# Performance work log

Hardware: AMD Instinct MI355X
Metric: run time of the kernel (lower is better)

## Reference

```python
import jax, jax.numpy as jnp
import numpy as np

EMBED, HIDDEN, VOCAB = 256, 512, 32000
B, T = 16, 63  # captions length; total steps per item = T+1


def setup_inputs() -> dict:
    key = jax.random.key(0)
    ks = jax.random.split(key, 9)
    s = 0.05
    return {
        "features": jax.random.normal(ks[0], (B, EMBED), jnp.float32),
        "captions": jax.random.randint(ks[1], (B, T), 0, VOCAB, jnp.int32),
        "emb": jax.random.normal(ks[2], (VOCAB, EMBED), jnp.float32) * s,
        "W_ih": jax.random.normal(ks[3], (4 * HIDDEN, EMBED), jnp.float32) * s,
        "W_hh": jax.random.normal(ks[4], (4 * HIDDEN, HIDDEN), jnp.float32) * s,
        "b_ih": jax.random.normal(ks[5], (4 * HIDDEN,), jnp.float32) * s,
        "b_hh": jax.random.normal(ks[6], (4 * HIDDEN,), jnp.float32) * s,
        "W_out": jax.random.normal(ks[7], (VOCAB, HIDDEN), jnp.float32) * s,
        "b_out": jax.random.normal(ks[8], (VOCAB,), jnp.float32) * s,
    }


def reference(features, captions, emb, W_ih, W_hh, b_ih, b_hh, W_out, b_out):
    H = W_hh.shape[1]
    embeds = emb[captions]  # [B, T, E]
    # inputs = cat(features.unsqueeze(1), embeds, dim=1) -> [B, T+1, E]
    inputs = jnp.concatenate([features[:, None, :], embeds], axis=1)
    # The torch loop threads self.hidden across batch items -> one long
    # sequential LSTM over B*(T+1) steps starting from zero state.
    xs = inputs.reshape(-1, inputs.shape[-1])  # [B*(T+1), E]
    # precompute input projections for all steps (one big GEMM)
    x_proj = xs @ W_ih.T + b_ih + b_hh  # [S, 4H]

    def cell(carry, xp):
        h, c = carry
        gates = xp + h @ W_hh.T  # [4H]
        i, f, g, o = jnp.split(gates, 4)
        i = jax.nn.sigmoid(i)
        f = jax.nn.sigmoid(f)
        g = jnp.tanh(g)
        o = jax.nn.sigmoid(o)
        c = f * c + i * g
        h = o * jnp.tanh(c)
        return (h, c), h

    h0 = jnp.zeros((H,), xs.dtype)
    c0 = jnp.zeros((H,), xs.dtype)
    _, hs = jax.lax.scan(cell, (h0, c0), x_proj)  # [S, H]
    logits = hs @ W_out.T + b_out  # [S, V]
    probs = jax.nn.softmax(logits, axis=-1)
    return probs.reshape(inputs.shape[0], inputs.shape[1], -1)  # [B, T+1, V]
```

## Files before the change

kernel.cpp:

```cpp
#include <hip/hip_runtime.h>
#include <cstdint>
#include <cstddef>

#define EMBED  256
#define HIDDEN 512
#define VOCAB  32000
#define BATCH  16
#define TCAP   63
#define STEPS  1024
#define GROWS  2048

#define WS_HBUF  0
#define WS_HS32  8192
#define WS_HSBF  2105344
#define WS_WB    3153920
#define WS_XPOFF (24u * 1024u * 1024u)
#define WS_NEED  36708352ull
#define WB_HEAD_ELEMS 12582912

typedef __bf16 bf16x8 __attribute__((ext_vector_type(8)));
typedef float  f32x4  __attribute__((ext_vector_type(4)));

__device__ __forceinline__ float sigmoid_f(float x) {
    return 1.0f / (1.0f + __expf(-x));
}
__device__ __forceinline__ float tanh_f(float x) {
    float a = fabsf(x);
    float e = __expf(-2.0f * a);
    float r = (1.0f - e) / (1.0f + e);
    return copysignf(r, x);
}
__device__ __forceinline__ float sel4(float a0, float a1, float a2, float a3, int j) {
    float lo = (j & 1) ? a1 : a0;
    float hi = (j & 1) ? a3 : a2;
    return (j & 2) ? hi : lo;
}
__device__ __forceinline__ unsigned short f2bf_u16(float f) {
    union { float f; unsigned u; } v; v.f = f;
    unsigned r = v.u + 0x7fffu + ((v.u >> 16) & 1u);
    return (unsigned short)(r >> 16);
}

__global__ __launch_bounds__(256) void xproj_kernel(
    const float* __restrict__ features,
    const int*   __restrict__ captions,
    const float* __restrict__ emb,
    const float* __restrict__ W_ih,
    const float* __restrict__ b_ih,
    const float* __restrict__ b_hh,
    float* __restrict__ xp)
{
    __shared__ float As[64][65];
    __shared__ float Bs[64][65];
    const int tid = threadIdx.x;
    const int tx = tid & 15, ty = tid >> 4;
    const int r0 = blockIdx.x * 64;
    const int s0 = blockIdx.y * 64;
    float accv[4][4] = {};

    for (int k0 = 0; k0 < EMBED; k0 += 64) {
#pragma unroll
        for (int i = 0; i < 4; ++i) {
            const int idx = tid + i * 256;
            const int row = idx >> 4, q = idx & 15;
            const int s = s0 + row, sb = s >> 6, st = s & 63;
            const float* xr = (st == 0)
                ? (features + (size_t)sb * EMBED)
                : (emb + (size_t)captions[sb * TCAP + st - 1] * EMBED);
            const float4 a = *(const float4*)(xr + k0 + q * 4);
            As[row][q * 4 + 0] = a.x; As[row][q * 4 + 1] = a.y;
            As[row][q * 4 + 2] = a.z; As[row][q * 4 + 3] = a.w;
            const float4 b = *(const float4*)(W_ih + (size_t)(r0 + row) * EMBED + k0 + q * 4);
            Bs[row][q * 4 + 0] = b.x; Bs[row][q * 4 + 1] = b.y;
            Bs[row][q * 4 + 2] = b.z; Bs[row][q * 4 + 3] = b.w;
        }
        __syncthreads();
#pragma unroll 16
        for (int kk = 0; kk < 64; ++kk) {
            float av[4], bv[4];
#pragma unroll
            for (int i = 0; i < 4; ++i) av[i] = As[ty * 4 + i][kk];
#pragma unroll
            for (int j = 0; j < 4; ++j) bv[j] = Bs[tx * 4 + j][kk];
#pragma unroll
            for (int i = 0; i < 4; ++i)
#pragma unroll
                for (int j = 0; j < 4; ++j)
                    accv[i][j] = fmaf(av[i], bv[j], accv[i][j]);
        }
        __syncthreads();
    }
#pragma unroll
    for (int j = 0; j < 4; ++j) {
        const int r = r0 + tx * 4 + j;
        const float bb = b_ih[r] + b_hh[r];
#pragma unroll
        for (int i = 0; i < 4; ++i)
            xp[(size_t)(s0 + ty * 4 + i) * GROWS + r] = accv[i][j] + bb;
    }
}

__global__ __launch_bounds__(256, 1) void lstm_scan_kernel(
    const float* __restrict__ W_hh,
    const float* __restrict__ xp,
    unsigned long long* __restrict__ hbuf,
    float* __restrict__ hs32,
    __bf16* __restrict__ hsbf,
    const float* __restrict__ W_out,
    unsigned short* __restrict__ Wb,
    const int wbf)
{
    const int tid = threadIdx.x;

    if (blockIdx.x >= 32) {
        const int cb = blockIdx.x - 32;
        const int stride = 224 * 256 * 4;
        for (int i = (cb * 256 + tid) * 4; i < WB_HEAD_ELEMS; i += stride) {
            const float4 v = *(const float4*)(W_out + i);
            ushort4 o;
            o.x = f2bf_u16(v.x); o.y = f2bf_u16(v.y);
            o.z = f2bf_u16(v.z); o.w = f2bf_u16(v.w);
            *(ushort4*)(Wb + i) = o;
        }
        return;
    }

    const int rg  = tid >> 6;
    const int kc  = tid & 63;
    const int w   = blockIdx.x * 4 + rg;
    const int j0  = w * 4;

    __shared__ float hlds[2][HIDDEN];

    const int t_own  = ((kc & 1) << 1) | ((kc >> 1) & 1);
    const int jj_own = (((kc >> 2) & 1) << 1) | ((kc >> 3) & 1);
    const int row_own = t_own * HIDDEN + j0 + jj_own;

    float Whh[4][4][8];
#pragma unroll
    for (int t = 0; t < 4; ++t) {
#pragma unroll
        for (int jj = 0; jj < 4; ++jj) {
            const int row = t * HIDDEN + j0 + jj;
            const float4* ph = (const float4*)(W_hh + (size_t)row * HIDDEN + kc * 8);
            const float4 h0 = ph[0], h1 = ph[1];
            Whh[t][jj][0] = h0.x; Whh[t][jj][1] = h0.y; Whh[t][jj][2] = h0.z; Whh[t][jj][3] = h0.w;
            Whh[t][jj][4] = h1.x; Whh[t][jj][5] = h1.y; Whh[t][jj][6] = h1.z; Whh[t][jj][7] = h1.w;
        }
    }

    float c_state = 0.0f;
    float xpv_next = xp[row_own];
    const int qi = rg * 128 + kc * 2;

    for (int s = 0; s < STEPS; ++s) {
        const int p = s & 1;
        const unsigned expect = (unsigned)s;
        const float xpv = xpv_next;

        const int sn = (s + 1 < STEPS) ? (s + 1) : (STEPS - 1);
        xpv_next = xp[(size_t)sn * GROWS + row_own];

        const unsigned long long* hb = hbuf + (size_t)p * HIDDEN + qi;
        unsigned long long va, vb;
        for (;;) {
            va = __hip_atomic_load(hb,     __ATOMIC_RELAXED, __HIP_MEMORY_SCOPE_AGENT);
            vb = __hip_atomic_load(hb + 1, __ATOMIC_RELAXED, __HIP_MEMORY_SCOPE_AGENT);
            const bool ok = ((unsigned)(va >> 32) == expect) &
                            ((unsigned)(vb >> 32) == expect);
            if (__all((int)ok)) break;
            __builtin_amdgcn_s_sleep(1);
        }
        hlds[p][qi]     = __uint_as_float((unsigned)(va & 0xffffffffULL));
        hlds[p][qi + 1] = __uint_as_float((unsigned)(vb & 0xffffffffULL));
        __syncthreads();

        float hreg[8];
        {
            const float4 a = *(const float4*)&hlds[p][kc * 8];
            const float4 b = *(const float4*)&hlds[p][kc * 8 + 4];
            hreg[0] = a.x; hreg[1] = a.y; hreg[2] = a.z; hreg[3] = a.w;
            hreg[4] = b.x; hreg[5] = b.y; hreg[6] = b.z; hreg[7] = b.w;
        }

        float acc[16];
#pragma unroll
        for (int t = 0; t < 4; ++t) {
#pragma unroll
            for (int jj = 0; jj < 4; ++jj) {
                float a = Whh[t][jj][0] * hreg[0];
#pragma unroll
                for (int kk = 1; kk < 8; ++kk)
                    a = fmaf(Whh[t][jj][kk], hreg[kk], a);
                acc[t * 4 + jj] = a;
            }
        }

#pragma unroll
        for (int i = 0; i < 8; ++i) {
            const float send = (kc & 1) ? acc[i] : acc[i + 8];
            const float keep = (kc & 1) ? acc[i + 8] : acc[i];
            acc[i] = keep + __shfl_xor(send, 1, 64);
        }
#pragma unroll
        for (int i = 0; i < 4; ++i) {
            const float send = (kc & 2) ? acc[i] : acc[i + 4];
            const float keep = (kc & 2) ? acc[i + 4] : acc[i];
            acc[i] = keep + __shfl_xor(send, 2, 64);
        }
#pragma unroll
        for (int i = 0; i < 2; ++i) {
            const float send = (kc & 4) ? acc[i] : acc[i + 2];
            const float keep = (kc & 4) ? acc[i + 2] : acc[i];
            acc[i] = keep + __shfl_xor(send, 4, 64);
        }
        {
            const float send = (kc & 8) ? acc[0] : acc[1];
            const float keep = (kc & 8) ? acc[1] : acc[0];
            acc[0] = keep + __shfl_xor(send, 8, 64);
        }
        float a = acc[0];
        a += __shfl_xor(a, 16, 64);
        a += __shfl_xor(a, 32, 64);
        a += xpv;

        const float g00 = a;
        const float g01 = __shfl_xor(a, 1, 64);
        const float g10 = __shfl_xor(a, 2, 64);
        const float g11 = __shfl_xor(g01, 2, 64);
        float gi = sel4(g00, g10, g01, g11, t_own);
        float gf = sel4(g00, g10, g01, g11, t_own ^ 1);
        float gg = sel4(g00, g10, g01, g11, t_own ^ 2);
        float go = sel4(g00, g10, g01, g11, t_own ^ 3);

        gi = sigmoid_f(gi);
        gf = sigmoid_f(gf);
        gg = tanh_f(gg);
        go = sigmoid_f(go);
        c_state = gf * c_state + gi * gg;
        const float hnew = go * tanh_f(c_state);

        if ((kc & 0x33) == 0) {
            const int j = j0 + jj_own;
            const unsigned long long pack =
                ((unsigned long long)(unsigned)(s + 1) << 32) |
                (unsigned long long)__float_as_uint(hnew);
            __hip_atomic_store(hbuf + (size_t)((s + 1) & 1) * HIDDEN + j, pack,
                               __ATOMIC_RELAXED, __HIP_MEMORY_SCOPE_AGENT);
            hs32[(size_t)s * HIDDEN + j] = hnew;
            if (wbf) hsbf[(size_t)s * HIDDEN + j] = (__bf16)hnew;
        }
    }
}

__global__ __launch_bounds__(256) void convert_tail_kernel(
    const float* __restrict__ W, unsigned short* __restrict__ Wb,
    int lo, int n)
{
    const int stride = gridDim.x * blockDim.x * 4;
    for (int i = lo + (blockIdx.x * blockDim.x + threadIdx.x) * 4; i < n; i += stride) {
        const float4 v = *(const float4*)(W + i);
        ushort4 o;
        o.x = f2bf_u16(v.x); o.y = f2bf_u16(v.y);
        o.z = f2bf_u16(v.z); o.w = f2bf_u16(v.w);
        *(ushort4*)(Wb + i) = o;
    }
}

__global__ __launch_bounds__(256) void logits_mfma_kernel(
    const __bf16* __restrict__ A,
    const __bf16* __restrict__ B,
    const float* __restrict__ b_out,
    float* __restrict__ out)
{
    __shared__ char AsR[16384];
    __shared__ char BsR[16384];
    const int tid  = threadIdx.x;
    const int lane = tid & 63;
    const int wave = tid >> 6;
    const int wm = (wave >> 1) * 64;
    const int wn = (wave & 1) * 64;
    const int n0 = blockIdx.x * 128;
    const int m0 = blockIdx.y * 128;

    f32x4 acc[4][4] = {};

    for (int k0 = 0; k0 < HIDDEN; k0 += 64) {
        if (k0) __syncthreads();
#pragma unroll
        for (int i = 0; i < 4; ++i) {
            const int o   = (tid + i * 256) << 4;
            const int row = o >> 7;
            const int cb  = o & 127;
            const int sc  = cb ^ ((row & 7) << 4);
            const bf16x8 av = *(const bf16x8*)(A + (size_t)(m0 + row) * HIDDEN + k0 + (cb >> 1));
            const bf16x8 bv = *(const bf16x8*)(B + (size_t)(n0 + row) * HIDDEN + k0 + (cb >> 1));
            *(bf16x8*)(AsR + row * 128 + sc) = av;
            *(bf16x8*)(BsR + row * 128 + sc) = bv;
        }
        __syncthreads();
#pragma unroll
        for (int ks = 0; ks < 2; ++ks) {
            const int kb = ks * 64 + ((lane >> 4) << 4);
            bf16x8 af[4], bfr[4];
#pragma unroll
            for (int mi = 0; mi < 4; ++mi) {
                const int r = wm + mi * 16 + (lane & 15);
                af[mi] = *(const bf16x8*)(AsR + r * 128 + (kb ^ ((r & 7) << 4)));
            }
#pragma unroll
            for (int ni = 0; ni < 4; ++ni) {
                const int r = wn + ni * 16 + (lane & 15);
                bfr[ni] = *(const bf16x8*)(BsR + r * 128 + (kb ^ ((r & 7) << 4)));
            }
#pragma unroll
            for (int mi = 0; mi < 4; ++mi)
#pragma unroll
                for (int ni = 0; ni < 4; ++ni)
                    acc[mi][ni] = __builtin_amdgcn_mfma_f32_16x16x32_bf16(
                        af[mi], bfr[ni], acc[mi][ni], 0, 0, 0);
        }
    }

#pragma unroll
    for (int ni = 0; ni < 4; ++ni) {
        const int col = n0 + wn + ni * 16 + (lane & 15);
        const float bo = b_out[col];
#pragma unroll
        for (int mi = 0; mi < 4; ++mi) {
            const int r0 = m0 + wm + mi * 16 + ((lane >> 4) << 2);
#pragma unroll
            for (int qq = 0; qq < 4; ++qq)
                out[(size_t)(r0 + qq) * VOCAB + col] = acc[mi][ni][qq] + bo;
        }
    }
}

__global__ __launch_bounds__(256) void logits_kernel(
    const float* __restrict__ hs,
    const float* __restrict__ W_out,
    const float* __restrict__ b_out,
    float* __restrict__ out)
{
    __shared__ float As[64][65];
    __shared__ float Bs[64][65];
    const int tid = threadIdx.x;
    const int tx = tid & 15, ty = tid >> 4;
    const int v0 = blockIdx.x * 64;
    const int s0 = blockIdx.y * 64;
    float accv[4][4] = {};

    for (int k0 = 0; k0 < HIDDEN; k0 += 64) {
#pragma unroll
        for (int i = 0; i < 4; ++i) {
            const int idx = tid + i * 256;
            const int r = idx >> 4, q = idx & 15;
            const float4 a = *(const float4*)(hs + (size_t)(s0 + r) * HIDDEN + k0 + q * 4);
            As[r][q * 4 + 0] = a.x; As[r][q * 4 + 1] = a.y;
            As[r][q * 4 + 2] = a.z; As[r][q * 4 + 3] = a.w;
            const float4 b = *(const float4*)(W_out + (size_t)(v0 + r) * HIDDEN + k0 + q * 4);
            Bs[r][q * 4 + 0] = b.x; Bs[r][q * 4 + 1] = b.y;
            Bs[r][q * 4 + 2] = b.z; Bs[r][q * 4 + 3] = b.w;
        }
        __syncthreads();
#pragma unroll 16
        for (int kk = 0; kk < 64; ++kk) {
            float av[4], bv[4];
#pragma unroll
            for (int i = 0; i < 4; ++i) av[i] = As[ty * 4 + i][kk];
#pragma unroll
            for (int j = 0; j < 4; ++j) bv[j] = Bs[tx * 4 + j][kk];
#pragma unroll
            for (int i = 0; i < 4; ++i)
#pragma unroll
                for (int j = 0; j < 4; ++j)
                    accv[i][j] = fmaf(av[i], bv[j], accv[i][j]);
        }
        __syncthreads();
    }
#pragma unroll
    for (int i = 0; i < 4; ++i) {
        const int s = s0 + ty * 4 + i;
#pragma unroll
        for (int j = 0; j < 4; ++j) {
            const int v = v0 + tx * 4 + j;
            out[(size_t)s * VOCAB + v] = accv[i][j] + b_out[v];
        }
    }
}

__global__ __launch_bounds__(256) void softmax_kernel(float* __restrict__ out)
{
    const int row = blockIdx.x;
    float* p = out + (size_t)row * VOCAB;
    const int tid = threadIdx.x;
    __shared__ float redm[4];
    __shared__ float reds[4];

    float m = -3.402823466e38f;
    for (int idx = tid * 4; idx < VOCAB; idx += 1024) {
        const float4 v = *(const float4*)(p + idx);
        m = fmaxf(m, fmaxf(fmaxf(v.x, v.y), fmaxf(v.z, v.w)));
    }
#pragma unroll
    for (int d = 1; d < 64; d <<= 1) m = fmaxf(m, __shfl_xor(m, d, 64));
    if ((tid & 63) == 0) redm[tid >> 6] = m;
    __syncthreads();
    m = fmaxf(fmaxf(redm[0], redm[1]), fmaxf(redm[2], redm[3]));

    float sum = 0.f;
    for (int idx = tid * 4; idx < VOCAB; idx += 1024) {
        const float4 v = *(const float4*)(p + idx);
        sum += __expf(v.x - m) + __expf(v.y - m) + __expf(v.z - m) + __expf(v.w - m);
    }
#pragma unroll
    for (int d = 1; d < 64; d <<= 1) sum += __shfl_xor(sum, d, 64);
    if ((tid & 63) == 0) reds[tid >> 6] = sum;
    __syncthreads();
    sum = reds[0] + reds[1] + reds[2] + reds[3];
    const float inv = 1.0f / sum;

    for (int idx = tid * 4; idx < VOCAB; idx += 1024) {
        const float4 v = *(const float4*)(p + idx);
        float4 o;
        o.x = __expf(v.x - m) * inv;
        o.y = __expf(v.y - m) * inv;
        o.z = __expf(v.z - m) * inv;
        o.w = __expf(v.w - m) * inv;
        *(float4*)(p + idx) = o;
    }
}

extern "C" void kernel_launch(void* const* d_in, const int* in_sizes, int n_in,
                              void* d_out, int out_size, void* d_ws, size_t ws_size,
                              hipStream_t stream)
{
    const float* features = (const float*)d_in[0];
    const int*   captions = (const int*)d_in[1];
    const float* emb      = (const float*)d_in[2];
    const float* W_ih     = (const float*)d_in[3];
    const float* W_hh     = (const float*)d_in[4];
    const float* b_ih     = (const float*)d_in[5];
    const float* b_hh     = (const float*)d_in[6];
    const float* W_out    = (const float*)d_in[7];
    const float* b_out    = (const float*)d_in[8];
    float* out = (float*)d_out;

    char* ws = (char*)d_ws;
    unsigned long long* hbuf = (unsigned long long*)(ws + WS_HBUF);
    float*              hs32 = (float*)(ws + WS_HS32);
    __bf16*             hsbf = (__bf16*)(ws + WS_HSBF);
    __bf16*             Wb   = (__bf16*)(ws + WS_WB);
    const bool mfma_ok = ws_size >= WS_NEED;
    float* xpb = mfma_ok ? (float*)(ws + WS_WB + WS_XPOFF) : (float*)(ws + WS_WB);

    hipMemsetAsync(d_ws, 0, 8192, stream);

    xproj_kernel<<<dim3(GROWS / 64, STEPS / 64), 256, 0, stream>>>(
        features, captions, emb, W_ih, b_ih, b_hh, xpb);

    lstm_scan_kernel<<<mfma_ok ? 256 : 32, 256, 0, stream>>>(
        W_hh, xpb, hbuf, hs32, hsbf,
        W_out, (unsigned short*)Wb, mfma_ok ? 1 : 0);

    if (mfma_ok) {
        convert_tail_kernel<<<512, 256, 0, stream>>>(
            W_out, (unsigned short*)Wb, WB_HEAD_ELEMS, VOCAB * HIDDEN);
        logits_mfma_kernel<<<dim3(VOCAB / 128, STEPS / 128), 256, 0, stream>>>(
            hsbf, Wb, b_out, out);
    } else {
        logits_kernel<<<dim3(VOCAB / 64, STEPS / 64), 256, 0, stream>>>(
            hs32, W_out, b_out, out);
    }
    softmax_kernel<<<STEPS, 256, 0, stream>>>(out);
}
```

Baseline: 2.170 ms.

## Co-locate LSTM scan blocks on one XCD and use L2-local fast handoff

Scan blocks are now assigned dynamically. Blocks that start on XCD 0 claim the 32 recurrent slots first, so all scan workgroups can share one L2 cache. When every slot holder sits on the same XCD, hidden-state exchange goes through a separate buffer using plain vectorized loads with sc0 and volatile stores. This avoids device-scope atomic round trips, and a bounded spin falls back to the agent-scope atomic buffer. The change depends on non-portable hardware register reads and L2 coherence assumptions, and it adds a startup rendezvous. The fp32 hidden-state store is skipped when the bf16 path is active.

```diff
diff --git a/kernel.cpp b/kernel.cpp
--- a/kernel.cpp
+++ b/kernel.cpp
@@ -9,17 +9,21 @@
 #define TCAP   63
 #define STEPS  1024
 #define GROWS  2048
-
-#define WS_HBUF  0
-#define WS_HS32  8192
-#define WS_HSBF  2105344
-#define WS_WB    3153920
+#define NCONV  224
+
+#define WS_FAST  0
+#define WS_SLOW  8192
+#define WS_CTRS  16384
+#define WS_HS32  16640
+#define WS_HSBF  (16640 + 2097152)
+#define WS_WB    (16640 + 3145728)
 #define WS_XPOFF (24u * 1024u * 1024u)
-#define WS_NEED  36708352ull
+#define WS_NEED  (3162368ull + 33554432ull)
 #define WB_HEAD_ELEMS 12582912
 
 typedef __bf16 bf16x8 __attribute__((ext_vector_type(8)));
 typedef float  f32x4  __attribute__((ext_vector_type(4)));
+typedef unsigned int u32x4v __attribute__((ext_vector_type(4)));
 
 __device__ __forceinline__ float sigmoid_f(float x) {
     return 1.0f / (1.0f + __expf(-x));
@@ -103,7 +107,9 @@
 __global__ __launch_bounds__(256, 1) void lstm_scan_kernel(
     const float* __restrict__ W_hh,
     const float* __restrict__ xp,
-    unsigned long long* __restrict__ hbuf,
+    unsigned long long* __restrict__ fastb,
+    unsigned long long* __restrict__ slowb,
+    unsigned* __restrict__ ctrs,
     float* __restrict__ hs32,
     __bf16* __restrict__ hsbf,
     const float* __restrict__ W_out,
@@ -111,11 +117,57 @@
     const int wbf)
 {
     const int tid = threadIdx.x;
-
-    if (blockIdx.x >= 32) {
-        const int cb = blockIdx.x - 32;
-        const int stride = 224 * 256 * 4;
-        for (int i = (cb * 256 + tid) * 4; i < WB_HEAD_ELEMS; i += stride) {
+    __shared__ int sh_slot, sh_uni, sh_ticket;
+
+    if (tid == 0) {
+        unsigned xcd;
+        asm volatile("s_getreg_b32 %0, hwreg(HW_REG_XCC_ID)" : "=s"(xcd));
+        int id = -1;
+        if (xcd == 0u) {
+            const unsigned c = __hip_atomic_fetch_add(ctrs + 0, 1u,
+                __ATOMIC_RELAXED, __HIP_MEMORY_SCOPE_AGENT);
+            if (c < 32u) id = (int)c;
+        }
+        if (id < 0) {
+            for (int t = 0; t < 24; ++t) {
+                if (__hip_atomic_load(ctrs + 0, __ATOMIC_RELAXED,
+                                      __HIP_MEMORY_SCOPE_AGENT) >= 32u) break;
+                __builtin_amdgcn_s_sleep(127);
+            }
+            if (__hip_atomic_load(ctrs + 0, __ATOMIC_RELAXED,
+                                  __HIP_MEMORY_SCOPE_AGENT) < 32u) {
+                const unsigned c = __hip_atomic_fetch_add(ctrs + 0, 1u,
+                    __ATOMIC_RELAXED, __HIP_MEMORY_SCOPE_AGENT);
+                if (c < 32u) id = (int)c;
+            }
+        }
+        int uni = 0;
+        if (id >= 0) {
+            __hip_atomic_fetch_add(ctrs + 1, 1u | ((xcd == 0u) ? 0u : 0x10000u),
+                                   __ATOMIC_RELAXED, __HIP_MEMORY_SCOPE_AGENT);
+            unsigned cd;
+            for (;;) {
+                cd = __hip_atomic_load(ctrs + 1, __ATOMIC_RELAXED,
+                                       __HIP_MEMORY_SCOPE_AGENT);
+                if ((cd & 0xffffu) >= 32u) break;
+                __builtin_amdgcn_s_sleep(2);
+            }
+            uni = ((cd >> 16) == 0u) ? 1 : 0;
+        } else {
+            sh_ticket = (int)__hip_atomic_fetch_add(ctrs + 2, 1u,
+                __ATOMIC_RELAXED, __HIP_MEMORY_SCOPE_AGENT);
+        }
+        sh_slot = id;
+        sh_uni = uni;
+    }
+    __syncthreads();
+    const int slot = sh_slot;
+
+    if (slot < 0) {
+        if (!wbf) return;
+        const int ticket = sh_ticket;
+        const int stride = NCONV * 256 * 4;
+        for (int i = (ticket * 256 + tid) * 4; i < WB_HEAD_ELEMS; i += stride) {
             const float4 v = *(const float4*)(W_out + i);
             ushort4 o;
             o.x = f2bf_u16(v.x); o.y = f2bf_u16(v.y);
@@ -125,9 +177,11 @@
         return;
     }
 
+    bool usefast = (sh_uni != 0);
+
     const int rg  = tid >> 6;
     const int kc  = tid & 63;
-    const int w   = blockIdx.x * 4 + rg;
+    const int w   = slot * 4 + rg;
     const int j0  = w * 4;
 
     __shared__ float hlds[2][HIDDEN];
@@ -161,18 +215,36 @@
         const int sn = (s + 1 < STEPS) ? (s + 1) : (STEPS - 1);
         xpv_next = xp[(size_t)sn * GROWS + row_own];
 
-        const unsigned long long* hb = hbuf + (size_t)p * HIDDEN + qi;
-        unsigned long long va, vb;
-        for (;;) {
-            va = __hip_atomic_load(hb,     __ATOMIC_RELAXED, __HIP_MEMORY_SCOPE_AGENT);
-            vb = __hip_atomic_load(hb + 1, __ATOMIC_RELAXED, __HIP_MEMORY_SCOPE_AGENT);
-            const bool ok = ((unsigned)(va >> 32) == expect) &
-                            ((unsigned)(vb >> 32) == expect);
-            if (__all((int)ok)) break;
-            __builtin_amdgcn_s_sleep(1);
-        }
-        hlds[p][qi]     = __uint_as_float((unsigned)(va & 0xffffffffULL));
-        hlds[p][qi + 1] = __uint_as_float((unsigned)(vb & 0xffffffffULL));
+        unsigned d0, d1;
+        const unsigned long long fa = (unsigned long long)(fastb + (size_t)p * HIDDEN + qi);
+        if (usefast) {
+            int it = 0;
+            for (;;) {
+                u32x4v v;
+                asm volatile("global_load_dwordx4 %0, %1, off sc0\n\t"
+                             "s_waitcnt vmcnt(0)"
+                             : "=v"(v) : "v"(fa) : "memory");
+                const bool ok = (v.y == expect) & (v.w == expect);
+                if (__all((int)ok)) { d0 = v.x; d1 = v.z; break; }
+                if (++it >= 2048) { usefast = false; break; }
+            }
+        }
+        if (!usefast) {
+            const unsigned long long* hb = slowb + (size_t)p * HIDDEN + qi;
+            unsigned long long va, vb;
+            for (;;) {
+                va = __hip_atomic_load(hb,     __ATOMIC_RELAXED, __HIP_MEMORY_SCOPE_AGENT);
+                vb = __hip_atomic_load(hb + 1, __ATOMIC_RELAXED, __HIP_MEMORY_SCOPE_AGENT);
+                const bool ok = ((unsigned)(va >> 32) == expect) &
+                                ((unsigned)(vb >> 32) == expect);
+                if (__all((int)ok)) break;
+                __builtin_amdgcn_s_sleep(1);
+            }
+            d0 = (unsigned)(va & 0xffffffffULL);
+            d1 = (unsigned)(vb & 0xffffffffULL);
+        }
+        hlds[p][qi]     = __uint_as_float(d0);
+        hlds[p][qi + 1] = __uint_as_float(d1);
         __syncthreads();
 
         float hreg[8];
@@ -240,15 +312,17 @@
         c_state = gf * c_state + gi * gg;
         const float hnew = go * tanh_f(c_state);
 
+        const int q = (s + 1) & 1;
         if ((kc & 0x33) == 0) {
             const int j = j0 + jj_own;
             const unsigned long long pack =
                 ((unsigned long long)(unsigned)(s + 1) << 32) |
                 (unsigned long long)__float_as_uint(hnew);
-            __hip_atomic_store(hbuf + (size_t)((s + 1) & 1) * HIDDEN + j, pack,
+            *(volatile unsigned long long*)(fastb + (size_t)q * HIDDEN + j) = pack;
+            __hip_atomic_store(slowb + (size_t)q * HIDDEN + j, pack,
                                __ATOMIC_RELAXED, __HIP_MEMORY_SCOPE_AGENT);
-            hs32[(size_t)s * HIDDEN + j] = hnew;
             if (wbf) hsbf[(size_t)s * HIDDEN + j] = (__bf16)hnew;
+            else     hs32[(size_t)s * HIDDEN + j] = hnew;
         }
     }
 }
@@ -447,20 +521,22 @@
     float* out = (float*)d_out;
 
     char* ws = (char*)d_ws;
-    unsigned long long* hbuf = (unsigned long long*)(ws + WS_HBUF);
-    float*              hs32 = (float*)(ws + WS_HS32);
-    __bf16*             hsbf = (__bf16*)(ws + WS_HSBF);
-    __bf16*             Wb   = (__bf16*)(ws + WS_WB);
+    unsigned long long* fastb = (unsigned long long*)(ws + WS_FAST);
+    unsigned long long* slowb = (unsigned long long*)(ws + WS_SLOW);
+    unsigned*           ctrs  = (unsigned*)(ws + WS_CTRS);
+    float*              hs32  = (float*)(ws + WS_HS32);
+    __bf16*             hsbf  = (__bf16*)(ws + WS_HSBF);
+    __bf16*             Wb    = (__bf16*)(ws + WS_WB);
     const bool mfma_ok = ws_size >= WS_NEED;
     float* xpb = mfma_ok ? (float*)(ws + WS_WB + WS_XPOFF) : (float*)(ws + WS_WB);
 
-    hipMemsetAsync(d_ws, 0, 8192, stream);
+    hipMemsetAsync(d_ws, 0, WS_HS32, stream);
 
     xproj_kernel<<<dim3(GROWS / 64, STEPS / 64), 256, 0, stream>>>(
         features, captions, emb, W_ih, b_ih, b_hh, xpb);
 
-    lstm_scan_kernel<<<mfma_ok ? 256 : 32, 256, 0, stream>>>(
-        W_hh, xpb, hbuf, hs32, hsbf,
+    lstm_scan_kernel<<<256, 256, 0, stream>>>(
+        W_hh, xpb, fastb, slowb, ctrs, hs32, hsbf,
         W_out, (unsigned short*)Wb, mfma_ok ? 1 : 0);
 
     if (mfma_ok) {
```

New measurement: 2.414 ms. 1.11x slower.

## Replicate per-block hidden-state mailboxes and move weight conversion into xproj kernel

Applied to the files above, without the earlier changes.

The LSTM scan now has each block poll its own replicated copy of the hidden-state buffer using one 16-byte cache-bypassing load. Previously all 32 blocks polled a shared 2-slot buffer with two atomic loads and a sleep. Producers write each value to two mailbox replicas via lane shuffles, so the stores are spread across lanes. The W_out bf16 head conversion moves from extra scan-kernel blocks into extra blocks of the input-projection kernel, so the scan runs without co-resident converter traffic. This aims to cut per-step sync latency and memory contention on the serial critical path, at the cost of more store traffic per step and inline asm relying on sc0/sc1 coherence semantics.

```diff
diff --git a/kernel.cpp b/kernel.cpp
--- a/kernel.cpp
+++ b/kernel.cpp
@@ -10,16 +10,17 @@
 #define STEPS  1024
 #define GROWS  2048
 
-#define WS_HBUF  0
-#define WS_HS32  8192
-#define WS_HSBF  2105344
-#define WS_WB    3153920
+#define WS_PBUF  0
+#define WS_HSBF  262144
+#define WS_HS32  1310720
+#define WS_WB    3407872
 #define WS_XPOFF (24u * 1024u * 1024u)
-#define WS_NEED  36708352ull
+#define WS_NEED  36962304ull
 #define WB_HEAD_ELEMS 12582912
 
 typedef __bf16 bf16x8 __attribute__((ext_vector_type(8)));
 typedef float  f32x4  __attribute__((ext_vector_type(4)));
+typedef unsigned int u32x4v __attribute__((ext_vector_type(4)));
 
 __device__ __forceinline__ float sigmoid_f(float x) {
     return 1.0f / (1.0f + __expf(-x));
@@ -35,24 +36,47 @@
     float hi = (j & 1) ? a3 : a2;
     return (j & 2) ? hi : lo;
 }
+__device__ __forceinline__ int sel4i(int a0, int a1, int a2, int a3, int j) {
+    int lo = (j & 1) ? a1 : a0;
+    int hi = (j & 1) ? a3 : a2;
+    return (j & 2) ? hi : lo;
+}
 __device__ __forceinline__ unsigned short f2bf_u16(float f) {
     union { float f; unsigned u; } v; v.f = f;
     unsigned r = v.u + 0x7fffu + ((v.u >> 16) & 1u);
     return (unsigned short)(r >> 16);
 }
 
-__global__ __launch_bounds__(256) void xproj_kernel(
+__global__ __launch_bounds__(256) void xproj_conv_kernel(
     const float* __restrict__ features,
     const int*   __restrict__ captions,
     const float* __restrict__ emb,
     const float* __restrict__ W_ih,
     const float* __restrict__ b_ih,
     const float* __restrict__ b_hh,
-    float* __restrict__ xp)
-{
+    float* __restrict__ xp,
+    const float* __restrict__ W_out,
+    unsigned short* __restrict__ Wb,
+    const int wbf)
+{
+    const int tid = threadIdx.x;
+
+    if (blockIdx.y >= 16) {
+        if (!wbf) return;
+        const int cid = (blockIdx.y - 16) * 32 + blockIdx.x;
+        const int stride = 256 * 256 * 4;
+        for (int i = (cid * 256 + tid) * 4; i < WB_HEAD_ELEMS; i += stride) {
+            const float4 v = *(const float4*)(W_out + i);
+            ushort4 o;
+            o.x = f2bf_u16(v.x); o.y = f2bf_u16(v.y);
+            o.z = f2bf_u16(v.z); o.w = f2bf_u16(v.w);
+            *(ushort4*)(Wb + i) = o;
+        }
+        return;
+    }
+
     __shared__ float As[64][65];
     __shared__ float Bs[64][65];
-    const int tid = threadIdx.x;
     const int tx = tid & 15, ty = tid >> 4;
     const int r0 = blockIdx.x * 64;
     const int s0 = blockIdx.y * 64;
@@ -103,31 +127,16 @@
 __global__ __launch_bounds__(256, 1) void lstm_scan_kernel(
     const float* __restrict__ W_hh,
     const float* __restrict__ xp,
-    unsigned long long* __restrict__ hbuf,
+    unsigned long long* __restrict__ pbuf,
     float* __restrict__ hs32,
     __bf16* __restrict__ hsbf,
-    const float* __restrict__ W_out,
-    unsigned short* __restrict__ Wb,
     const int wbf)
 {
     const int tid = threadIdx.x;
-
-    if (blockIdx.x >= 32) {
-        const int cb = blockIdx.x - 32;
-        const int stride = 224 * 256 * 4;
-        for (int i = (cb * 256 + tid) * 4; i < WB_HEAD_ELEMS; i += stride) {
-            const float4 v = *(const float4*)(W_out + i);
-            ushort4 o;
-            o.x = f2bf_u16(v.x); o.y = f2bf_u16(v.y);
-            o.z = f2bf_u16(v.z); o.w = f2bf_u16(v.w);
-            *(ushort4*)(Wb + i) = o;
-        }
-        return;
-    }
-
     const int rg  = tid >> 6;
     const int kc  = tid & 63;
-    const int w   = blockIdx.x * 4 + rg;
+    const int g   = blockIdx.x;
+    const int w   = g * 4 + rg;
     const int j0  = w * 4;
 
     __shared__ float hlds[2][HIDDEN];
@@ -135,6 +144,12 @@
     const int t_own  = ((kc & 1) << 1) | ((kc >> 1) & 1);
     const int jj_own = (((kc >> 2) & 1) << 1) | ((kc >> 3) & 1);
     const int row_own = t_own * HIDDEN + j0 + jj_own;
+
+    const int e_pub = kc & 3;
+    const int src_lane = sel4i(0, 8, 4, 12, e_pub);
+    const int c0 = kc >> 2;
+    unsigned long long* const mc0 = pbuf + (size_t)c0 * 2 * HIDDEN + j0 + e_pub;
+    unsigned long long* const mc1 = mc0 + (size_t)16 * 2 * HIDDEN;
 
     float Whh[4][4][8];
 #pragma unroll
@@ -150,29 +165,29 @@
     }
 
     float c_state = 0.0f;
-    float xpv_next = xp[row_own];
+    float xpv = xp[row_own];
+    float xpv_next;
     const int qi = rg * 128 + kc * 2;
 
     for (int s = 0; s < STEPS; ++s) {
         const int p = s & 1;
         const unsigned expect = (unsigned)s;
-        const float xpv = xpv_next;
-
-        const int sn = (s + 1 < STEPS) ? (s + 1) : (STEPS - 1);
-        xpv_next = xp[(size_t)sn * GROWS + row_own];
-
-        const unsigned long long* hb = hbuf + (size_t)p * HIDDEN + qi;
-        unsigned long long va, vb;
+
+        const unsigned long long fa =
+            (unsigned long long)(pbuf + ((size_t)g * 2 + p) * HIDDEN + qi);
+        unsigned d0, d1;
         for (;;) {
-            va = __hip_atomic_load(hb,     __ATOMIC_RELAXED, __HIP_MEMORY_SCOPE_AGENT);
-            vb = __hip_atomic_load(hb + 1, __ATOMIC_RELAXED, __HIP_MEMORY_SCOPE_AGENT);
-            const bool ok = ((unsigned)(va >> 32) == expect) &
-                            ((unsigned)(vb >> 32) == expect);
-            if (__all((int)ok)) break;
-            __builtin_amdgcn_s_sleep(1);
-        }
-        hlds[p][qi]     = __uint_as_float((unsigned)(va & 0xffffffffULL));
-        hlds[p][qi + 1] = __uint_as_float((unsigned)(vb & 0xffffffffULL));
+            u32x4v v;
+            asm volatile("global_load_dwordx4 %0, %1, off sc0 sc1\n\t"
+                         "s_waitcnt vmcnt(0)"
+                         : "=&v"(v) : "v"(fa) : "memory");
+            if (__all((int)((v.y == expect) & (v.w == expect)))) {
+                d0 = v.x; d1 = v.z; break;
+            }
+        }
+
+        hlds[p][qi]     = __uint_as_float(d0);
+        hlds[p][qi + 1] = __uint_as_float(d1);
         __syncthreads();
 
         float hreg[8];
@@ -182,6 +197,9 @@
             hreg[0] = a.x; hreg[1] = a.y; hreg[2] = a.z; hreg[3] = a.w;
             hreg[4] = b.x; hreg[5] = b.y; hreg[6] = b.z; hreg[7] = b.w;
         }
+
+        const int sn = (s + 1 < STEPS) ? (s + 1) : (STEPS - 1);
+        xpv_next = xp[(size_t)sn * GROWS + row_own];
 
         float acc[16];
 #pragma unroll
@@ -240,16 +258,23 @@
         c_state = gf * c_state + gi * gg;
         const float hnew = go * tanh_f(c_state);
 
+        const int q = (s + 1) & 1;
+        const float hsrc = __shfl(hnew, src_lane, 64);
+        const unsigned long long pack =
+            ((unsigned long long)(unsigned)(s + 1) << 32) |
+            (unsigned long long)__float_as_uint(hsrc);
+        __hip_atomic_store(mc0 + (size_t)q * HIDDEN, pack,
+                           __ATOMIC_RELAXED, __HIP_MEMORY_SCOPE_AGENT);
+        __hip_atomic_store(mc1 + (size_t)q * HIDDEN, pack,
+                           __ATOMIC_RELAXED, __HIP_MEMORY_SCOPE_AGENT);
+
         if ((kc & 0x33) == 0) {
             const int j = j0 + jj_own;
-            const unsigned long long pack =
-                ((unsigned long long)(unsigned)(s + 1) << 32) |
-                (unsigned long long)__float_as_uint(hnew);
-            __hip_atomic_store(hbuf + (size_t)((s + 1) & 1) * HIDDEN + j, pack,
-                               __ATOMIC_RELAXED, __HIP_MEMORY_SCOPE_AGENT);
-            hs32[(size_t)s * HIDDEN + j] = hnew;
             if (wbf) hsbf[(size_t)s * HIDDEN + j] = (__bf16)hnew;
-        }
+            else     hs32[(size_t)s * HIDDEN + j] = hnew;
+        }
+
+        xpv = xpv_next;
     }
 }
 
@@ -447,21 +472,21 @@
     float* out = (float*)d_out;
 
     char* ws = (char*)d_ws;
-    unsigned long long* hbuf = (unsigned long long*)(ws + WS_HBUF);
+    unsigned long long* pbuf = (unsigned long long*)(ws + WS_PBUF);
+    __bf16*             hsbf = (__bf16*)(ws + WS_HSBF);
     float*              hs32 = (float*)(ws + WS_HS32);
-    __bf16*             hsbf = (__bf16*)(ws + WS_HSBF);
     __bf16*             Wb   = (__bf16*)(ws + WS_WB);
     const bool mfma_ok = ws_size >= WS_NEED;
     float* xpb = mfma_ok ? (float*)(ws + WS_WB + WS_XPOFF) : (float*)(ws + WS_WB);
 
-    hipMemsetAsync(d_ws, 0, 8192, stream);
-
-    xproj_kernel<<<dim3(GROWS / 64, STEPS / 64), 256, 0, stream>>>(
-        features, captions, emb, W_ih, b_ih, b_hh, xpb);
-
-    lstm_scan_kernel<<<mfma_ok ? 256 : 32, 256, 0, stream>>>(
-        W_hh, xpb, hbuf, hs32, hsbf,
+    hipMemsetAsync(d_ws, 0, 32 * 2 * HIDDEN * 8, stream);
+
+    xproj_conv_kernel<<<dim3(32, 24), 256, 0, stream>>>(
+        features, captions, emb, W_ih, b_ih, b_hh, xpb,
         W_out, (unsigned short*)Wb, mfma_ok ? 1 : 0);
+
+    lstm_scan_kernel<<<32, 256, 0, stream>>>(
+        W_hh, xpb, pbuf, hs32, hsbf, mfma_ok ? 1 : 0);
 
     if (mfma_ok) {
         convert_tail_kernel<<<512, 256, 0, stream>>>(
```

After: 2.349 ms. +8.2%, slower.
